# Kernel tuning notes

Hardware: AMD Instinct MI355X
Metric: run time of the kernel (lower is better)

Reference implementation:

```python
import jax, jax.numpy as jnp
import numpy as np

N_NODES = 50000
IN_CH = 256
HID_CH = 64
N_EDGES = 800000


def setup_inputs() -> dict:
    key = jax.random.key(0)
    k1, k2, k3, k4, k5 = jax.random.split(key, 5)
    x = jax.random.normal(k1, (N_NODES, IN_CH), dtype=jnp.float32)
    edge_index = jax.random.randint(k2, (2, N_EDGES), 0, N_NODES, dtype=jnp.int64)
    # GCNConv linear weight (Glorot) and zero bias, as in PyG defaults
    W = jax.random.normal(k3, (IN_CH, HID_CH), dtype=jnp.float32) * (1.0 / np.sqrt(IN_CH))
    bias = jnp.zeros((HID_CH,), dtype=jnp.float32)
    # PReLU per-channel weight, torch default init 0.25
    prelu_a = jnp.full((HID_CH,), 0.25, dtype=jnp.float32)
    return {"x": x, "edge_index": edge_index, "W": W, "bias": bias, "prelu_a": prelu_a}


def reference(x, edge_index, W, bias, prelu_a):
    # GCNConv, normalize=False: transform then scatter-add over edges, + bias
    xw = x @ W                               # [N, H]
    src, dst = edge_index[0], edge_index[1]
    msgs = xw[src]                           # [E, H] gather
    agg = jax.ops.segment_sum(msgs, dst, num_segments=N_NODES)  # [N, H]
    out = agg + bias
    # per-channel PReLU
    return jnp.where(out > 0, out, prelu_a * out)
```

## Files before the change

### kernel.cpp

```cpp
#include <hip/hip_runtime.h>

#define N_NODES 50000
#define IN_CH   256
#define HID_CH  64
#define N_EDGES 800000

#define AG_ROWS 64
#define NBUCKET 782
#define CAPB    1536
#define PTILE   4096
#define NPT     196
#define GEMM_BLOCKS 391
#define CAP     2048

typedef __attribute__((ext_vector_type(8))) short short8;
typedef __attribute__((ext_vector_type(4))) float f32x4;

static __device__ __forceinline__ unsigned short f2bf(float f) {
    unsigned int u = __float_as_uint(f);
    u += 0x7FFF + ((u >> 16) & 1);
    return (unsigned short)(u >> 16);
}
static __device__ __forceinline__ float bf2f(unsigned short h) {
    return __uint_as_float(((unsigned int)h) << 16);
}

__global__ __launch_bounds__(256) void wfrag_kernel(const float* __restrict__ W,
                                                    unsigned short* __restrict__ wfrag,
                                                    int* __restrict__ cnt) {
    const int idx = blockIdx.x * 256 + threadIdx.x;
    if (idx < NBUCKET) cnt[idx] = 0;
    if (idx >= 2048) return;
    const int ks = idx >> 8;
    const int nt = (idx >> 6) & 3;
    const int l  = idx & 63;
    const int q = l >> 4, m = l & 15;
    const int n = nt * 16 + m;
    const int k0 = ks * 32 + q * 8;
    short8 v;
    #pragma unroll
    for (int j = 0; j < 8; ++j) v[j] = (short)f2bf(W[(k0 + j) * HID_CH + n]);
    ((short8*)wfrag)[idx] = v;
}

__global__ __launch_bounds__(512) void gemm_part_kernel(const float* __restrict__ x,
                                                        const unsigned short* __restrict__ wfrag,
                                                        unsigned short* __restrict__ xwb,
                                                        const int* __restrict__ ei,
                                                        int* __restrict__ cnt,
                                                        unsigned int* __restrict__ packed_out) {
    __shared__ int hcnt[NBUCKET];
    __shared__ int excl[NBUCKET];
    __shared__ int lcur[NBUCKET];
    __shared__ int gbase[NBUCKET];
    __shared__ int wsum[8];
    __shared__ unsigned int staged[PTILE];
    __shared__ unsigned short sbkt[PTILE];

    const int t = threadIdx.x;

    if (blockIdx.x < GEMM_BLOCKS) {
        const int wv = t >> 6, lane = t & 63;
        const int q = lane >> 4, m = lane & 15;
        const int row0 = blockIdx.x * 128 + wv * 16;
        const int arow = row0 + m;
        const int arl = arow < N_NODES ? arow : N_NODES - 1;
        const float* xr = x + (size_t)arl * IN_CH + q * 8;
        const short8* wf = (const short8*)wfrag;

        f32x4 acc0 = {0.f,0.f,0.f,0.f}, acc1 = acc0, acc2 = acc0, acc3 = acc0;

        #pragma unroll
        for (int ks = 0; ks < 8; ++ks) {
            const float4 a0 = *(const float4*)(xr + ks * 32);
            const float4 a1 = *(const float4*)(xr + ks * 32 + 4);
            short8 af;
            af[0] = (short)f2bf(a0.x); af[1] = (short)f2bf(a0.y);
            af[2] = (short)f2bf(a0.z); af[3] = (short)f2bf(a0.w);
            af[4] = (short)f2bf(a1.x); af[5] = (short)f2bf(a1.y);
            af[6] = (short)f2bf(a1.z); af[7] = (short)f2bf(a1.w);
            const short8 b0 = wf[(ks * 4 + 0) * 64 + lane];
            const short8 b1 = wf[(ks * 4 + 1) * 64 + lane];
            const short8 b2 = wf[(ks * 4 + 2) * 64 + lane];
            const short8 b3 = wf[(ks * 4 + 3) * 64 + lane];
            acc0 = __builtin_amdgcn_mfma_f32_16x16x32_bf16(af, b0, acc0, 0, 0, 0);
            acc1 = __builtin_amdgcn_mfma_f32_16x16x32_bf16(af, b1, acc1, 0, 0, 0);
            acc2 = __builtin_amdgcn_mfma_f32_16x16x32_bf16(af, b2, acc2, 0, 0, 0);
            acc3 = __builtin_amdgcn_mfma_f32_16x16x32_bf16(af, b3, acc3, 0, 0, 0);
        }

        #pragma unroll
        for (int r = 0; r < 4; ++r) {
            const int row = row0 + q * 4 + r;
            if (row < N_NODES) {
                unsigned short* o = xwb + (size_t)row * HID_CH + m;
                o[0]  = f2bf(acc0[r]);
                o[16] = f2bf(acc1[r]);
                o[32] = f2bf(acc2[r]);
                o[48] = f2bf(acc3[r]);
            }
        }
        return;
    }

    const int tile0 = (blockIdx.x - GEMM_BLOCKS) * PTILE;
    const int tcnt = min(PTILE, N_EDGES - tile0);

    for (int i = t; i < NBUCKET; i += 512) hcnt[i] = 0;
    __syncthreads();

    int es[8], ed[8];
    #pragma unroll
    for (int r = 0; r < 2; ++r) {
        const int base = tile0 + (r * 512 + t) * 4;
        if (base < N_EDGES) {
            const int4 s4 = *(const int4*)(ei + base);
            const int4 d4 = *(const int4*)(ei + N_EDGES + base);
            es[r*4+0] = s4.x; es[r*4+1] = s4.y; es[r*4+2] = s4.z; es[r*4+3] = s4.w;
            ed[r*4+0] = d4.x; ed[r*4+1] = d4.y; ed[r*4+2] = d4.z; ed[r*4+3] = d4.w;
        } else {
            #pragma unroll
            for (int j = 0; j < 4; ++j) es[r*4+j] = -1;
        }
    }
    #pragma unroll
    for (int i = 0; i < 8; ++i)
        if (es[i] >= 0) atomicAdd(&hcnt[ed[i] >> 6], 1);
    __syncthreads();

    const int b0 = 2 * t, b1 = 2 * t + 1;
    const int c0 = (b0 < NBUCKET) ? hcnt[b0] : 0;
    const int c1 = (b1 < NBUCKET) ? hcnt[b1] : 0;
    const int v = c0 + c1;
    int s = v;
    #pragma unroll
    for (int off = 1; off < 64; off <<= 1) {
        const int u = __shfl_up(s, off, 64);
        if ((t & 63) >= off) s += u;
    }
    if ((t & 63) == 63) wsum[t >> 6] = s;
    __syncthreads();
    if (t < 8) {
        const int ws = wsum[t];
        int si = ws;
        #pragma unroll
        for (int off = 1; off < 8; off <<= 1) {
            const int u = __shfl_up(si, off, 64);
            if (t >= off) si += u;
        }
        wsum[t] = si - ws;
    }
    __syncthreads();
    const int ex = s - v + wsum[t >> 6];
    if (b0 < NBUCKET) {
        excl[b0] = ex; lcur[b0] = ex;
        if (c0 > 0) gbase[b0] = b0 * CAPB + atomicAdd(&cnt[b0], c0);
    }
    if (b1 < NBUCKET) {
        excl[b1] = ex + c0; lcur[b1] = ex + c0;
        if (c1 > 0) gbase[b1] = b1 * CAPB + atomicAdd(&cnt[b1], c1);
    }
    __syncthreads();

    #pragma unroll
    for (int i = 0; i < 8; ++i) {
        if (es[i] >= 0) {
            const int b = ed[i] >> 6;
            const int pos = atomicAdd(&lcur[b], 1);
            staged[pos] = ((unsigned int)(ed[i] & 63) << 16) | (unsigned int)es[i];
            sbkt[pos] = (unsigned short)b;
        }
    }
    __syncthreads();

    #pragma unroll
    for (int i = 0; i < 8; ++i) {
        const int idx = t + i * 512;
        if (idx < tcnt) {
            const int b = sbkt[idx];
            packed_out[gbase[b] + (idx - excl[b])] = staged[idx];
        }
    }
}

__global__ __launch_bounds__(512) void aggregate_kernel(const unsigned short* __restrict__ xwb,
                                                        const unsigned int* __restrict__ packed,
                                                        const int* __restrict__ cnt,
                                                        const float* __restrict__ bias,
                                                        const float* __restrict__ prelu_a,
                                                        float* __restrict__ out) {
    __shared__ unsigned short ssrc[CAP];
    __shared__ int hcnt[AG_ROWS];
    __shared__ int hexcl[AG_ROWS];
    __shared__ int hcur[AG_ROWS];
    __shared__ float acc[AG_ROWS * HID_CH];

    const int b = blockIdx.x;
    const int t = threadIdx.x;
    const int beg = b * CAPB;
    const int total = min(cnt[b], CAP);
    const int wv = t >> 6, lane = t & 63;
    const int slot = lane >> 4, c0 = (lane & 15) * 4;

    #pragma unroll
    for (int i = 0; i < 8; ++i) acc[t + i * 512] = 0.f;
    if (t < AG_ROWS) hcnt[t] = 0;
    __syncthreads();

    for (int i = t; i < total; i += 512)
        atomicAdd(&hcnt[packed[beg + i] >> 16], 1);
    __syncthreads();

    if (t < AG_ROWS) {
        const int v = hcnt[t];
        int s = v;
        #pragma unroll
        for (int off = 1; off < 64; off <<= 1) {
            const int u = __shfl_up(s, off, 64);
            if (t >= off) s += u;
        }
        hexcl[t] = s - v;
        hcur[t]  = s - v;
    }
    __syncthreads();

    for (int i = t; i < total; i += 512) {
        const unsigned int p = packed[beg + i];
        const int pos = atomicAdd(&hcur[p >> 16], 1);
        ssrc[pos] = (unsigned short)(p & 0xFFFFu);
    }
    __syncthreads();

    #pragma unroll
    for (int k = 0; k < 8; ++k) {
        const int nl = wv * 8 + k;
        const int rb = hexcl[nl];
        const int re = rb + hcnt[nl];
        float4 a4 = make_float4(0.f, 0.f, 0.f, 0.f);
        int i = rb + slot;
        for (; i + 12 < re; i += 16) {
            const int s0 = ssrc[i];
            const int s1 = ssrc[i + 4];
            const int s2 = ssrc[i + 8];
            const int s3 = ssrc[i + 12];
            const ushort4 v0 = *(const ushort4*)(xwb + (size_t)s0 * HID_CH + c0);
            const ushort4 v1 = *(const ushort4*)(xwb + (size_t)s1 * HID_CH + c0);
            const ushort4 v2 = *(const ushort4*)(xwb + (size_t)s2 * HID_CH + c0);
            const ushort4 v3 = *(const ushort4*)(xwb + (size_t)s3 * HID_CH + c0);
            a4.x += bf2f(v0.x) + bf2f(v1.x) + bf2f(v2.x) + bf2f(v3.x);
            a4.y += bf2f(v0.y) + bf2f(v1.y) + bf2f(v2.y) + bf2f(v3.y);
            a4.z += bf2f(v0.z) + bf2f(v1.z) + bf2f(v2.z) + bf2f(v3.z);
            a4.w += bf2f(v0.w) + bf2f(v1.w) + bf2f(v2.w) + bf2f(v3.w);
        }
        for (; i < re; i += 4) {
            const int s = ssrc[i];
            const ushort4 v = *(const ushort4*)(xwb + (size_t)s * HID_CH + c0);
            a4.x += bf2f(v.x); a4.y += bf2f(v.y);
            a4.z += bf2f(v.z); a4.w += bf2f(v.w);
        }
        a4.x += __shfl_xor(a4.x, 16, 64); a4.y += __shfl_xor(a4.y, 16, 64);
        a4.z += __shfl_xor(a4.z, 16, 64); a4.w += __shfl_xor(a4.w, 16, 64);
        a4.x += __shfl_xor(a4.x, 32, 64); a4.y += __shfl_xor(a4.y, 32, 64);
        a4.z += __shfl_xor(a4.z, 32, 64); a4.w += __shfl_xor(a4.w, 32, 64);
        if (slot == 0) {
            float4* ap = (float4*)&acc[nl * HID_CH + c0];
            float4 c4 = *ap;
            c4.x += a4.x; c4.y += a4.y; c4.z += a4.z; c4.w += a4.w;
            *ap = c4;
        }
    }
    __syncthreads();

    const int node0 = b * AG_ROWS;
    const int nrows = min(AG_ROWS, N_NODES - node0);
    for (int i = t; i < nrows * (HID_CH / 4); i += 512) {
        const int r = i >> 4;
        const int cc = (i & 15) * 4;
        const float4 a4 = *(float4*)&acc[r * HID_CH + cc];
        const float4 bb = *(const float4*)(bias + cc);
        const float4 aa = *(const float4*)(prelu_a + cc);
        float4 rr;
        rr.x = a4.x + bb.x; rr.x = rr.x > 0.f ? rr.x : aa.x * rr.x;
        rr.y = a4.y + bb.y; rr.y = rr.y > 0.f ? rr.y : aa.y * rr.y;
        rr.z = a4.z + bb.z; rr.z = rr.z > 0.f ? rr.z : aa.z * rr.z;
        rr.w = a4.w + bb.w; rr.w = rr.w > 0.f ? rr.w : aa.w * rr.w;
        *(float4*)(out + (size_t)(node0 + r) * HID_CH + cc) = rr;
    }
}

extern "C" void kernel_launch(void* const* d_in, const int* in_sizes, int n_in,
                              void* d_out, int out_size, void* d_ws, size_t ws_size,
                              hipStream_t stream) {
    const float* x       = (const float*)d_in[0];
    const int*   ei      = (const int*)d_in[1];
    const float* W       = (const float*)d_in[2];
    const float* bias    = (const float*)d_in[3];
    const float* prelu_a = (const float*)d_in[4];
    float* out = (float*)d_out;

    char* w = (char*)d_ws;
    unsigned short* xwb    = (unsigned short*)(w);
    int*            cnt    = (int*)(w + 6400000);
    unsigned int*   packed = (unsigned int*)(w + 6403200);
    unsigned short* wfrag  = (unsigned short*)(w + 11207808);

    wfrag_kernel<<<8, 256, 0, stream>>>(W, wfrag, cnt);

    gemm_part_kernel<<<GEMM_BLOCKS + NPT, 512, 0, stream>>>(x, wfrag, xwb, ei, cnt, packed);

    aggregate_kernel<<<NBUCKET, 512, 0, stream>>>(xwb, packed, cnt, bias, prelu_a, out);
}
```

Before: 130.3 us.

## Fuse W fragment prep into GEMM, restructure aggregation to one row per 8 threads

Drops the separate wfrag kernel. Each GEMM block now converts W to bf16 MFMA fragments in shared memory, unioned with the partition scratch, and the counter reset becomes a hipMemsetAsync. The aggregate kernel no longer splits each node across four slots with shuffle reduction and a shared fp32 accumulator. Eight threads now own one node's 64 channels, each loading 16-byte short8 rows and writing bias+PReLU output directly. This removes a kernel launch, the shared-accumulator round trip and the shuffles, at the cost of redundant W conversion in every GEMM block and a serial per-node loop that is less balanced across high-degree nodes.

```diff
diff --git a/kernel.cpp b/kernel.cpp
--- a/kernel.cpp
+++ b/kernel.cpp
@@ -25,48 +25,49 @@
     return __uint_as_float(((unsigned int)h) << 16);
 }
 
-__global__ __launch_bounds__(256) void wfrag_kernel(const float* __restrict__ W,
-                                                    unsigned short* __restrict__ wfrag,
-                                                    int* __restrict__ cnt) {
-    const int idx = blockIdx.x * 256 + threadIdx.x;
-    if (idx < NBUCKET) cnt[idx] = 0;
-    if (idx >= 2048) return;
-    const int ks = idx >> 8;
-    const int nt = (idx >> 6) & 3;
-    const int l  = idx & 63;
-    const int q = l >> 4, m = l & 15;
-    const int n = nt * 16 + m;
-    const int k0 = ks * 32 + q * 8;
-    short8 v;
-    #pragma unroll
-    for (int j = 0; j < 8; ++j) v[j] = (short)f2bf(W[(k0 + j) * HID_CH + n]);
-    ((short8*)wfrag)[idx] = v;
-}
+union SmemU {
+    short8 wfl[2048];
+    struct {
+        int hcnt[NBUCKET];
+        int excl[NBUCKET];
+        int lcur[NBUCKET];
+        int gbase[NBUCKET];
+        int wsum[8];
+        unsigned int staged[PTILE];
+        unsigned short sbkt[PTILE];
+    } p;
+};
 
 __global__ __launch_bounds__(512) void gemm_part_kernel(const float* __restrict__ x,
-                                                        const unsigned short* __restrict__ wfrag,
+                                                        const float* __restrict__ W,
                                                         unsigned short* __restrict__ xwb,
                                                         const int* __restrict__ ei,
                                                         int* __restrict__ cnt,
                                                         unsigned int* __restrict__ packed_out) {
-    __shared__ int hcnt[NBUCKET];
-    __shared__ int excl[NBUCKET];
-    __shared__ int lcur[NBUCKET];
-    __shared__ int gbase[NBUCKET];
-    __shared__ int wsum[8];
-    __shared__ unsigned int staged[PTILE];
-    __shared__ unsigned short sbkt[PTILE];
-
+    __shared__ SmemU u;
     const int t = threadIdx.x;
 
     if (blockIdx.x < GEMM_BLOCKS) {
+        for (int e = t; e < 2048; e += 512) {
+            const int ks = e >> 8;
+            const int nt = (e >> 6) & 3;
+            const int l  = e & 63;
+            const int q = l >> 4, m = l & 15;
+            const int n = nt * 16 + m;
+            const int k0 = ks * 32 + q * 8;
+            short8 v;
+            #pragma unroll
+            for (int j = 0; j < 8; ++j) v[j] = (short)f2bf(W[(k0 + j) * HID_CH + n]);
+            u.wfl[e] = v;
+        }
+        __syncthreads();
+
         const int wv = t >> 6, lane = t & 63;
         const int q = lane >> 4, m = lane & 15;
         const int row0 = blockIdx.x * 128 + wv * 16;
         const int arow = row0 + m;
         const int arl = arow < N_NODES ? arow : N_NODES - 1;
         const float* xr = x + (size_t)arl * IN_CH + q * 8;
-        const short8* wf = (const short8*)wfrag;
 
         f32x4 acc0 = {0.f,0.f,0.f,0.f}, acc1 = acc0, acc2 = acc0, acc3 = acc0;
 
@@ -79,10 +80,10 @@
             af[2] = (short)f2bf(a0.z); af[3] = (short)f2bf(a0.w);
             af[4] = (short)f2bf(a1.x); af[5] = (short)f2bf(a1.y);
             af[6] = (short)f2bf(a1.z); af[7] = (short)f2bf(a1.w);
-            const short8 b0 = wf[(ks * 4 + 0) * 64 + lane];
-            const short8 b1 = wf[(ks * 4 + 1) * 64 + lane];
-            const short8 b2 = wf[(ks * 4 + 2) * 64 + lane];
-            const short8 b3 = wf[(ks * 4 + 3) * 64 + lane];
+            const short8 b0 = u.wfl[(ks * 4 + 0) * 64 + lane];
+            const short8 b1 = u.wfl[(ks * 4 + 1) * 64 + lane];
+            const short8 b2 = u.wfl[(ks * 4 + 2) * 64 + lane];
+            const short8 b3 = u.wfl[(ks * 4 + 3) * 64 + lane];
             acc0 = __builtin_amdgcn_mfma_f32_16x16x32_bf16(af, b0, acc0, 0, 0, 0);
             acc1 = __builtin_amdgcn_mfma_f32_16x16x32_bf16(af, b1, acc1, 0, 0, 0);
             acc2 = __builtin_amdgcn_mfma_f32_16x16x32_bf16(af, b2, acc2, 0, 0, 0);
@@ -106,7 +107,7 @@
     const int tile0 = (blockIdx.x - GEMM_BLOCKS) * PTILE;
     const int tcnt = min(PTILE, N_EDGES - tile0);
 
-    for (int i = t; i < NBUCKET; i += 512) hcnt[i] = 0;
+    for (int i = t; i < NBUCKET; i += 512) u.p.hcnt[i] = 0;
     __syncthreads();
 
     int es[8], ed[8];
@@ -125,40 +126,40 @@
     }
     #pragma unroll
     for (int i = 0; i < 8; ++i)
-        if (es[i] >= 0) atomicAdd(&hcnt[ed[i] >> 6], 1);
+        if (es[i] >= 0) atomicAdd(&u.p.hcnt[ed[i] >> 6], 1);
     __syncthreads();
 
     const int b0 = 2 * t, b1 = 2 * t + 1;
-    const int c0 = (b0 < NBUCKET) ? hcnt[b0] : 0;
-    const int c1 = (b1 < NBUCKET) ? hcnt[b1] : 0;
+    const int c0 = (b0 < NBUCKET) ? u.p.hcnt[b0] : 0;
+    const int c1 = (b1 < NBUCKET) ? u.p.hcnt[b1] : 0;
     const int v = c0 + c1;
     int s = v;
     #pragma unroll
     for (int off = 1; off < 64; off <<= 1) {
-        const int u = __shfl_up(s, off, 64);
-        if ((t & 63) >= off) s += u;
-    }
-    if ((t & 63) == 63) wsum[t >> 6] = s;
+        const int uu = __shfl_up(s, off, 64);
+        if ((t & 63) >= off) s += uu;
+    }
+    if ((t & 63) == 63) u.p.wsum[t >> 6] = s;
     __syncthreads();
     if (t < 8) {
-        const int ws = wsum[t];
+        const int ws = u.p.wsum[t];
         int si = ws;
         #pragma unroll
         for (int off = 1; off < 8; off <<= 1) {
-            const int u = __shfl_up(si, off, 64);
-            if (t >= off) si += u;
-        }
-        wsum[t] = si - ws;
-    }
-    __syncthreads();
-    const int ex = s - v + wsum[t >> 6];
+            const int uu = __shfl_up(si, off, 64);
+            if (t >= off) si += uu;
+        }
+        u.p.wsum[t] = si - ws;
+    }
+    __syncthreads();
+    const int ex = s - v + u.p.wsum[t >> 6];
     if (b0 < NBUCKET) {
-        excl[b0] = ex; lcur[b0] = ex;
-        if (c0 > 0) gbase[b0] = b0 * CAPB + atomicAdd(&cnt[b0], c0);
+        u.p.excl[b0] = ex; u.p.lcur[b0] = ex;
+        if (c0 > 0) u.p.gbase[b0] = b0 * CAPB + atomicAdd(&cnt[b0], c0);
     }
     if (b1 < NBUCKET) {
-        excl[b1] = ex + c0; lcur[b1] = ex + c0;
-        if (c1 > 0) gbase[b1] = b1 * CAPB + atomicAdd(&cnt[b1], c1);
+        u.p.excl[b1] = ex + c0; u.p.lcur[b1] = ex + c0;
+        if (c1 > 0) u.p.gbase[b1] = b1 * CAPB + atomicAdd(&cnt[b1], c1);
     }
     __syncthreads();
 
@@ -166,9 +167,9 @@
     for (int i = 0; i < 8; ++i) {
         if (es[i] >= 0) {
             const int b = ed[i] >> 6;
-            const int pos = atomicAdd(&lcur[b], 1);
-            staged[pos] = ((unsigned int)(ed[i] & 63) << 16) | (unsigned int)es[i];
-            sbkt[pos] = (unsigned short)b;
+            const int pos = atomicAdd(&u.p.lcur[b], 1);
+            u.p.staged[pos] = ((unsigned int)(ed[i] & 63) << 16) | (unsigned int)es[i];
+            u.p.sbkt[pos] = (unsigned short)b;
         }
     }
     __syncthreads();
@@ -177,8 +178,8 @@
     for (int i = 0; i < 8; ++i) {
         const int idx = t + i * 512;
         if (idx < tcnt) {
-            const int b = sbkt[idx];
-            packed_out[gbase[b] + (idx - excl[b])] = staged[idx];
+            const int b = u.p.sbkt[idx];
+            packed_out[u.p.gbase[b] + (idx - u.p.excl[b])] = u.p.staged[idx];
         }
     }
 }
@@ -193,17 +194,12 @@
     __shared__ int hcnt[AG_ROWS];
     __shared__ int hexcl[AG_ROWS];
     __shared__ int hcur[AG_ROWS];
-    __shared__ float acc[AG_ROWS * HID_CH];
 
     const int b = blockIdx.x;
     const int t = threadIdx.x;
     const int beg = b * CAPB;
     const int total = min(cnt[b], CAP);
-    const int wv = t >> 6, lane = t & 63;
-    const int slot = lane >> 4, c0 = (lane & 15) * 4;
-
-    #pragma unroll
-    for (int i = 0; i < 8; ++i) acc[t + i * 512] = 0.f;
+
     if (t < AG_ROWS) hcnt[t] = 0;
     __syncthreads();
 
@@ -231,60 +227,56 @@
     }
     __syncthreads();
 
-    #pragma unroll
-    for (int k = 0; k < 8; ++k) {
-        const int nl = wv * 8 + k;
-        const int rb = hexcl[nl];
-        const int re = rb + hcnt[nl];
-        float4 a4 = make_float4(0.f, 0.f, 0.f, 0.f);
-        int i = rb + slot;
-        for (; i + 12 < re; i += 16) {
-            const int s0 = ssrc[i];
-            const int s1 = ssrc[i + 4];
-            const int s2 = ssrc[i + 8];
-            const int s3 = ssrc[i + 12];
-            const ushort4 v0 = *(const ushort4*)(xwb + (size_t)s0 * HID_CH + c0);
-            const ushort4 v1 = *(const ushort4*)(xwb + (size_t)s1 * HID_CH + c0);
-            const ushort4 v2 = *(const ushort4*)(xwb + (size_t)s2 * HID_CH + c0);
-            const ushort4 v3 = *(const ushort4*)(xwb + (size_t)s3 * HID_CH + c0);
-            a4.x += bf2f(v0.x) + bf2f(v1.x) + bf2f(v2.x) + bf2f(v3.x);
-            a4.y += bf2f(v0.y) + bf2f(v1.y) + bf2f(v2.y) + bf2f(v3.y);
-            a4.z += bf2f(v0.z) + bf2f(v1.z) + bf2f(v2.z) + bf2f(v3.z);
-            a4.w += bf2f(v0.w) + bf2f(v1.w) + bf2f(v2.w) + bf2f(v3.w);
-        }
-        for (; i < re; i += 4) {
-            const int s = ssrc[i];
-            const ushort4 v = *(const ushort4*)(xwb + (size_t)s * HID_CH + c0);
-            a4.x += bf2f(v.x); a4.y += bf2f(v.y);
-            a4.z += bf2f(v.z); a4.w += bf2f(v.w);
-        }
-        a4.x += __shfl_xor(a4.x, 16, 64); a4.y += __shfl_xor(a4.y, 16, 64);
-        a4.z += __shfl_xor(a4.z, 16, 64); a4.w += __shfl_xor(a4.w, 16, 64);
-        a4.x += __shfl_xor(a4.x, 32, 64); a4.y += __shfl_xor(a4.y, 32, 64);
-        a4.z += __shfl_xor(a4.z, 32, 64); a4.w += __shfl_xor(a4.w, 32, 64);
-        if (slot == 0) {
-            float4* ap = (float4*)&acc[nl * HID_CH + c0];
-            float4 c4 = *ap;
-            c4.x += a4.x; c4.y += a4.y; c4.z += a4.z; c4.w += a4.w;
-            *ap = c4;
-        }
-    }
-    __syncthreads();
-
-    const int node0 = b * AG_ROWS;
-    const int nrows = min(AG_ROWS, N_NODES - node0);
-    for (int i = t; i < nrows * (HID_CH / 4); i += 512) {
-        const int r = i >> 4;
-        const int cc = (i & 15) * 4;
-        const float4 a4 = *(float4*)&acc[r * HID_CH + cc];
-        const float4 bb = *(const float4*)(bias + cc);
-        const float4 aa = *(const float4*)(prelu_a + cc);
-        float4 rr;
-        rr.x = a4.x + bb.x; rr.x = rr.x > 0.f ? rr.x : aa.x * rr.x;
-        rr.y = a4.y + bb.y; rr.y = rr.y > 0.f ? rr.y : aa.y * rr.y;
-        rr.z = a4.z + bb.z; rr.z = rr.z > 0.f ? rr.z : aa.z * rr.z;
-        rr.w = a4.w + bb.w; rr.w = rr.w > 0.f ? rr.w : aa.w * rr.w;
-        *(float4*)(out + (size_t)(node0 + r) * HID_CH + cc) = rr;
+    const int sl = t >> 3;
+    const int li = t & 7;
+    const int c0 = li * 8;
+    const int rb = hexcl[sl];
+    const int re = rb + hcnt[sl];
+
+    float a[8];
+    #pragma unroll
+    for (int j = 0; j < 8; ++j) a[j] = 0.f;
+
+    int i = rb;
+    for (; i + 3 < re; i += 4) {
+        const int e0 = ssrc[i + 0];
+        const int e1 = ssrc[i + 1];
+        const int e2 = ssrc[i + 2];
+        const int e3 = ssrc[i + 3];
+        const short8 v0 = *(const short8*)(xwb + (size_t)e0 * HID_CH + c0);
+        const short8 v1 = *(const short8*)(xwb + (size_t)e1 * HID_CH + c0);
+        const short8 v2 = *(const short8*)(xwb + (size_t)e2 * HID_CH + c0);
+        const short8 v3 = *(const short8*)(xwb + (size_t)e3 * HID_CH + c0);
+        #pragma unroll
+        for (int j = 0; j < 8; ++j)
+            a[j] += (bf2f((unsigned short)v0[j]) + bf2f((unsigned short)v1[j]))
+                  + (bf2f((unsigned short)v2[j]) + bf2f((unsigned short)v3[j]));
+    }
+    for (; i < re; ++i) {
+        const int e0 = ssrc[i];
+        const short8 v0 = *(const short8*)(xwb + (size_t)e0 * HID_CH + c0);
+        #pragma unroll
+        for (int j = 0; j < 8; ++j) a[j] += bf2f((unsigned short)v0[j]);
+    }
+
+    const int node = b * AG_ROWS + sl;
+    if (node < N_NODES) {
+        const float4 bb0 = *(const float4*)(bias + c0);
+        const float4 bb1 = *(const float4*)(bias + c0 + 4);
+        const float4 aa0 = *(const float4*)(prelu_a + c0);
+        const float4 aa1 = *(const float4*)(prelu_a + c0 + 4);
+        float4 r0, r1;
+        r0.x = a[0] + bb0.x; r0.x = r0.x > 0.f ? r0.x : aa0.x * r0.x;
+        r0.y = a[1] + bb0.y; r0.y = r0.y > 0.f ? r0.y : aa0.y * r0.y;
+        r0.z = a[2] + bb0.z; r0.z = r0.z > 0.f ? r0.z : aa0.z * r0.z;
+        r0.w = a[3] + bb0.w; r0.w = r0.w > 0.f ? r0.w : aa0.w * r0.w;
+        r1.x = a[4] + bb1.x; r1.x = r1.x > 0.f ? r1.x : aa1.x * r1.x;
+        r1.y = a[5] + bb1.y; r1.y = r1.y > 0.f ? r1.y : aa1.y * r1.y;
+        r1.z = a[6] + bb1.z; r1.z = r1.z > 0.f ? r1.z : aa1.z * r1.z;
+        r1.w = a[7] + bb1.w; r1.w = r1.w > 0.f ? r1.w : aa1.w * r1.w;
+        float4* op = (float4*)(out + (size_t)node * HID_CH + c0);
+        op[0] = r0;
+        op[1] = r1;
     }
 }
 
@@ -302,11 +294,10 @@
     unsigned short* xwb    = (unsigned short*)(w);
     int*            cnt    = (int*)(w + 6400000);
     unsigned int*   packed = (unsigned int*)(w + 6403200);
-    unsigned short* wfrag  = (unsigned short*)(w + 11207808);
-
-    wfrag_kernel<<<8, 256, 0, stream>>>(W, wfrag, cnt);
-
-    gemm_part_kernel<<<GEMM_BLOCKS + NPT, 512, 0, stream>>>(x, wfrag, xwb, ei, cnt, packed);
+
+    hipMemsetAsync(cnt, 0, NBUCKET * sizeof(int), stream);
+
+    gemm_part_kernel<<<GEMM_BLOCKS + NPT, 512, 0, stream>>>(x, W, xwb, ei, cnt, packed);
 
     aggregate_kernel<<<NBUCKET, 512, 0, stream>>>(xwb, packed, cnt, bias, prelu_a, out);
 }
```

New measurement: 125.4 us. 1.04x faster.
